# Optimization experiments

Hardware: AMD Instinct MI355X
Metric: run time of the kernel (lower is better)

## Reference

```python
import jax, jax.numpy as jnp
import numpy as np
import math

B, T, D, H, DM = 2, 2048, 1024, 16, 256
DK = D // H

def setup_inputs() -> dict:
    key = jax.random.key(0)
    ks = jax.random.split(key, 13)
    s = 0.02
    return {
        "Hx": jax.random.normal(ks[0], (B, D, T, 1), jnp.float32),
        "Hf": jax.random.normal(ks[1], (B, T, D), jnp.float32),
        "Gm": jax.random.normal(ks[2], (B, T, DM), jnp.float32),
        "Wg": jax.random.normal(ks[3], (T, DM), jnp.float32) * s,
        "bg": jax.random.normal(ks[4], (T,), jnp.float32) * s,
        "Wq": jax.random.normal(ks[5], (D, 2 * D), jnp.float32) * s,
        "bq": jax.random.normal(ks[6], (D,), jnp.float32) * s,
        "Wk": jax.random.normal(ks[7], (D, 2 * D), jnp.float32) * s,
        "bk": jax.random.normal(ks[8], (D,), jnp.float32) * s,
        "Wv": jax.random.normal(ks[9], (D, D), jnp.float32) * s,
        "bv": jax.random.normal(ks[10], (D,), jnp.float32) * s,
        "Wo": jax.random.normal(ks[11], (D, D), jnp.float32) * s,
        "bo": jax.random.normal(ks[12], (D,), jnp.float32) * s,
    }

def reference(Hx, Hf, Gm, Wg, bg, Wq, bq, Wk, bk, Wv, bv, Wo, bo):
    # Hx: (B, D, T, 1) -> (B, T, D)
    hx = jnp.transpose(Hx[..., 0], (0, 2, 1))
    h_cat = jnp.concatenate([hx, Hf], axis=-1)          # (B, T, 2D)
    Q = h_cat @ Wq.T + bq                               # (B, T, D)
    K = h_cat @ Wk.T + bk
    V = hx @ Wv.T + bv
    # split heads: (B, H, T, DK)
    Q = Q.reshape(B, T, H, DK).transpose(0, 2, 1, 3)
    K = K.reshape(B, T, H, DK).transpose(0, 2, 1, 3)
    V = V.reshape(B, T, H, DK).transpose(0, 2, 1, 3)
    scores = jnp.einsum('bhqd,bhkd->bhqk', Q, K) / math.sqrt(DK)
    bias = Gm @ Wg.T + bg                                # (B, T, T)
    scores = scores + bias[:, None, :, :]
    attn = jax.nn.softmax(scores, axis=-1)
    out = jnp.einsum('bhqk,bhkd->bhqd', attn, V)
    out = out.transpose(0, 2, 1, 3).reshape(B, T, D)
    return out @ Wo.T + bo
```

## Files before the change

### kernel.cpp

```cpp
#include <hip/hip_runtime.h>
#include <hip/hip_bf16.h>

using bf16 = __hip_bfloat16;
typedef __attribute__((ext_vector_type(8))) __bf16 bf16x8;
typedef __attribute__((ext_vector_type(4))) float f32x4;

#define GLB_AS(p) ((const __attribute__((address_space(1))) unsigned int*)(p))
#define LDS_AS(p) ((__attribute__((address_space(3))) unsigned int*)(p))

__device__ __forceinline__ void async_copy16(const void* g, void* l) {
  __builtin_amdgcn_global_load_lds(GLB_AS(g), LDS_AS(l), 16, 0, 0);
}

__device__ __forceinline__ f32x4 mfma16x16x32(bf16x8 a, bf16x8 b, f32x4 c) {
  return __builtin_amdgcn_mfma_f32_16x16x32_bf16(a, b, c, 0, 0, 0);
}

__device__ __forceinline__ float bfu2f(unsigned short u) {
  union { unsigned int i; float f; } x;
  x.i = (unsigned int)u << 16;
  return x.f;
}

#define LOG2E 1.44269504f

__global__ __launch_bounds__(256) void pack_hx(const float* __restrict__ Hx,
                                               bf16* __restrict__ hcat) {
  __shared__ float tile[64][65];
  const int t0 = blockIdx.x * 64, d0 = blockIdx.y * 64, b = blockIdx.z;
  const int c = threadIdx.x & 63, r0 = threadIdx.x >> 6;
#pragma unroll
  for (int i = 0; i < 16; ++i) {
    const int rd = r0 + i * 4;
    tile[rd][c] = Hx[((size_t)(b * 1024 + d0 + rd)) * 2048 + t0 + c];
  }
  __syncthreads();
#pragma unroll
  for (int i = 0; i < 16; ++i) {
    const int ct = r0 + i * 4;
    hcat[((size_t)(b * 2048 + t0 + ct)) * 2048 + d0 + c] =
        __float2bfloat16(tile[c][ct]);
  }
}

__global__ __launch_bounds__(256) void pack_all(
    const float* __restrict__ Hf, const float* __restrict__ Wq,
    const float* __restrict__ Wk, const float* __restrict__ Wv,
    const float* __restrict__ Wo, const float* __restrict__ Wg,
    const float* __restrict__ Gm, const float* __restrict__ bq,
    const float* __restrict__ bk, const float* __restrict__ bv,
    bf16* __restrict__ hcat, bf16* __restrict__ Wqkvb, bf16* __restrict__ Wob,
    bf16* __restrict__ Wgb, bf16* __restrict__ Gmb,
    float* __restrict__ qkvbias) {
  const int gid = blockIdx.x * 256 + threadIdx.x;
  const float* src = nullptr;
  bf16* dst = nullptr;
  int lg = 0, ldo = 0, off = 0, idx = 0;
  bool zero = false;
  if (gid < 1048576) { idx = gid; src = Hf; dst = hcat; lg = 8; ldo = 2048; off = 1024; }
  else if (gid < 1572864) { idx = gid - 1048576; src = Wq; dst = Wqkvb; lg = 9; ldo = 2048; }
  else if (gid < 2097152) { idx = gid - 1572864; src = Wk; dst = Wqkvb + (size_t)1024 * 2048; lg = 9; ldo = 2048; }
  else if (gid < 2359296) { idx = gid - 2097152; src = Wv; dst = Wqkvb + (size_t)2048 * 2048; lg = 8; ldo = 2048; }
  else if (gid < 2621440) { idx = gid - 2359296; zero = true; dst = Wqkvb + (size_t)2048 * 2048 + 1024; lg = 8; ldo = 2048; }
  else if (gid < 2883584) { idx = gid - 2621440; src = Wo; dst = Wob; lg = 8; ldo = 1024; }
  else if (gid < 3014656) { idx = gid - 2883584; src = Wg; dst = Wgb; lg = 6; ldo = 256; }
  else if (gid < 3276800) { idx = gid - 3014656; src = Gm; dst = Gmb; lg = 6; ldo = 256; }
  else if (gid < 3277056) { const int i = gid - 3276800; ((float4*)qkvbias)[i] = ((const float4*)bq)[i]; return; }
  else if (gid < 3277312) { const int i = gid - 3277056; ((float4*)(qkvbias + 1024))[i] = ((const float4*)bk)[i]; return; }
  else { const int i = gid - 3277312; ((float4*)(qkvbias + 2048))[i] = ((const float4*)bv)[i]; return; }
  const int row = idx >> lg, c = idx & ((1 << lg) - 1);
  bf16* o = dst + (size_t)row * ldo + off + c * 4;
  __align__(8) bf16 tmp[4];
  if (zero) {
    tmp[0] = tmp[1] = tmp[2] = tmp[3] = __float2bfloat16(0.f);
  } else {
    const float4 v = ((const float4*)src)[(size_t)idx];
    tmp[0] = __float2bfloat16(v.x); tmp[1] = __float2bfloat16(v.y);
    tmp[2] = __float2bfloat16(v.z); tmp[3] = __float2bfloat16(v.w);
  }
  *(ushort4*)o = *(const ushort4*)tmp;
}

__global__ __launch_bounds__(256) void gemm_qkv_bias(
    const bf16* __restrict__ hcat, const bf16* __restrict__ Wqkv,
    const float* __restrict__ qkvbias, const bf16* __restrict__ Gmb,
    const bf16* __restrict__ Wgb, const float* __restrict__ bg,
    bf16* __restrict__ QKb, bf16* __restrict__ Vt, bf16* __restrict__ biasS) {
  __shared__ __align__(16) bf16 As[128 * 64];
  __shared__ __align__(16) bf16 Bs[128 * 64];
  const bool isqkv = blockIdx.x < 24;
  const bf16* A = isqkv ? hcat : Gmb;
  const bf16* W = isqkv ? Wqkv : Wgb;
  const float* biasv = isqkv ? qkvbias : bg;
  const int Kd = isqkv ? 2048 : 256;
  const int n0 = (isqkv ? blockIdx.x : (blockIdx.x - 24)) * 128;
  const int m0 = blockIdx.y * 128;
  const int tid = threadIdx.x, lane = tid & 63, w = tid >> 6;
  const int wm = (w >> 1) * 64, wn = (w & 1) * 64;
  const int fr = lane & 15;
  const int ck = lane >> 4;

  f32x4 acc[4][4];
  const f32x4 fzero = {0.f, 0.f, 0.f, 0.f};
#pragma unroll
  for (int i = 0; i < 4; ++i)
#pragma unroll
    for (int j = 0; j < 4; ++j) acc[i][j] = fzero;

  for (int k0 = 0; k0 < Kd; k0 += 64) {
    __syncthreads();
#pragma unroll
    for (int is = 0; is < 4; ++is) {
      const int off = is * 4096 + w * 1024;
      const int row = (off >> 7) + (lane >> 3);
      const int sch = ((lane & 7) ^ (row & 7)) * 8;
      async_copy16(A + (size_t)(m0 + row) * Kd + k0 + sch, (char*)As + off);
      async_copy16(W + (size_t)(n0 + row) * Kd + k0 + sch, (char*)Bs + off);
    }
    __syncthreads();
#pragma unroll
    for (int ks = 0; ks < 2; ++ks) {
      bf16x8 af[4], bfr[4];
#pragma unroll
      for (int i = 0; i < 4; ++i) {
        const int swk = (((ks * 4 + ck) ^ (fr & 7))) * 8;
        af[i] = *(const bf16x8*)(As + (wm + i * 16 + fr) * 64 + swk);
        bfr[i] = *(const bf16x8*)(Bs + (wn + i * 16 + fr) * 64 + swk);
      }
#pragma unroll
      for (int i = 0; i < 4; ++i)
#pragma unroll
        for (int j = 0; j < 4; ++j)
          acc[i][j] = mfma16x16x32(af[i], bfr[j], acc[i][j]);
    }
  }
  const int erow = (lane >> 4) * 4;
  const int ecol = lane & 15;

  if (!isqkv) {
#pragma unroll
    for (int i = 0; i < 4; ++i) {
      const int gm0 = m0 + wm + i * 16 + erow;
#pragma unroll
      for (int j = 0; j < 4; ++j) {
        const int gn = n0 + wn + j * 16 + ecol;
        const float bv = biasv[gn];
#pragma unroll
        for (int r = 0; r < 4; ++r)
          biasS[(size_t)(gm0 + r) * 2048 + gn] =
              __float2bfloat16((acc[i][j][r] + bv) * LOG2E);
      }
    }
  } else if (n0 < 2048) {
    const float sc = (n0 < 1024) ? 0.125f * LOG2E : 1.0f;
#pragma unroll
    for (int i = 0; i < 4; ++i) {
      const int gm0 = m0 + wm + i * 16 + erow;
#pragma unroll
      for (int j = 0; j < 4; ++j) {
        const int gn = n0 + wn + j * 16 + ecol;
        const float bv = biasv[gn];
#pragma unroll
        for (int r = 0; r < 4; ++r)
          QKb[(size_t)(gm0 + r) * 2048 + gn] =
              __float2bfloat16((acc[i][j][r] + bv) * sc);
      }
    }
  } else {
#pragma unroll
    for (int i = 0; i < 4; ++i) {
      const int gm0 = m0 + wm + i * 16 + erow;
      const int bb = gm0 >> 11;
      const int t = gm0 & 2047;
#pragma unroll
      for (int j = 0; j < 4; ++j) {
        const int gn = n0 + wn + j * 16 + ecol;
        const float bv = biasv[gn];
        const int d = gn - 2048;
        __align__(8) bf16 tmp[4];
#pragma unroll
        for (int r = 0; r < 4; ++r)
          tmp[r] = __float2bfloat16(acc[i][j][r] + bv);
        *(ushort4*)(Vt + ((size_t)(bb * 1024 + d)) * 2048 + t) =
            *(const ushort4*)tmp;
      }
    }
  }
}

__global__ __launch_bounds__(256) void gemm_out(const bf16* __restrict__ A,
                                                const bf16* __restrict__ W,
                                                const float* __restrict__ biasv,
                                                float* __restrict__ C) {
  __shared__ __align__(16) bf16 As[128 * 64];
  __shared__ __align__(16) bf16 Bs[64 * 64];
  const int tid = threadIdx.x, lane = tid & 63, w = tid >> 6;
  const int m0 = blockIdx.y * 128, n0 = blockIdx.x * 64;
  const int wm = (w >> 1) * 64, wn = (w & 1) * 32;
  const int fr = lane & 15;
  const int ck = lane >> 4;

  f32x4 acc[4][2];
  const f32x4 fzero = {0.f, 0.f, 0.f, 0.f};
#pragma unroll
  for (int i = 0; i < 4; ++i)
#pragma unroll
    for (int j = 0; j < 2; ++j) acc[i][j] = fzero;

  for (int k0 = 0; k0 < 1024; k0 += 64) {
    __syncthreads();
#pragma unroll
    for (int is = 0; is < 4; ++is) {
      const int off = is * 4096 + w * 1024;
      const int row = (off >> 7) + (lane >> 3);
      const int sch = ((lane & 7) ^ (row & 7)) * 8;
      async_copy16(A + (size_t)(m0 + row) * 1024 + k0 + sch, (char*)As + off);
      if (is < 2)
        async_copy16(W + (size_t)(n0 + row) * 1024 + k0 + sch, (char*)Bs + off);
    }
    __syncthreads();
#pragma unroll
    for (int ks = 0; ks < 2; ++ks) {
      bf16x8 af[4], bfr[2];
      const int swk0 = (((ks * 4 + ck) ^ (fr & 7))) * 8;
#pragma unroll
      for (int i = 0; i < 4; ++i)
        af[i] = *(const bf16x8*)(As + (wm + i * 16 + fr) * 64 + swk0);
#pragma unroll
      for (int j = 0; j < 2; ++j)
        bfr[j] = *(const bf16x8*)(Bs + (wn + j * 16 + fr) * 64 + swk0);
#pragma unroll
      for (int i = 0; i < 4; ++i)
#pragma unroll
        for (int j = 0; j < 2; ++j)
          acc[i][j] = mfma16x16x32(af[i], bfr[j], acc[i][j]);
    }
  }
  const int erow = (lane >> 4) * 4;
  const int ecol = lane & 15;
#pragma unroll
  for (int i = 0; i < 4; ++i) {
    const int gm0 = m0 + wm + i * 16 + erow;
#pragma unroll
    for (int j = 0; j < 2; ++j) {
      const int gn = n0 + wn + j * 16 + ecol;
      const float bv = biasv[gn];
#pragma unroll
      for (int r = 0; r < 4; ++r)
        C[(size_t)(gm0 + r) * 1024 + gn] = acc[i][j][r] + bv;
    }
  }
}

__global__ __launch_bounds__(256) void flash_attn(
    const bf16* __restrict__ Qm, const bf16* __restrict__ Km,
    const bf16* __restrict__ Vtm, const bf16* __restrict__ biasS,
    bf16* __restrict__ Om) {
  __shared__ __align__(16) bf16 Ks[128 * 64];
  __shared__ __align__(16) bf16 Vs[64 * 128];
  __shared__ __align__(16) bf16 Ps[4 * 32 * 80];
  const int tid = threadIdx.x, lane = tid & 63, w = tid >> 6;
  const int q0 = blockIdx.x * 128;
  const int h = blockIdx.y, b = blockIdx.z;
  const int ql = lane & 15, qk = lane >> 4;
  const int T = 2048, D = 1024;

  bf16x8 qf[2][2];
#pragma unroll
  for (int qt = 0; qt < 2; ++qt)
#pragma unroll
    for (int ks = 0; ks < 2; ++ks)
      qf[qt][ks] = *(const bf16x8*)(
          Qm + (size_t)(b * T + q0 + w * 32 + qt * 16 + ql) * 2048 + h * 64 +
          ks * 32 + qk * 8);

  f32x4 acc[4][2];
  const f32x4 fzero = {0.f, 0.f, 0.f, 0.f};
#pragma unroll
  for (int dt = 0; dt < 4; ++dt)
#pragma unroll
    for (int qt = 0; qt < 2; ++qt) acc[dt][qt] = fzero;
  float lp[2] = {0.f, 0.f};

  const bf16* kbase = Km + (size_t)(b * T) * 2048 + h * 64;
  const bf16* vbase = Vtm + (size_t)(b * D + h * 64) * 2048;
  const bf16* bb0 = biasS + (size_t)(b * T + q0 + w * 32 + ql) * 2048 + qk * 4;
  bf16* pb = Ps + w * 2560;

  for (int j = 0; j < 16; ++j) {
    __syncthreads();
#pragma unroll
    for (int is = 0; is < 4; ++is) {
      const int off = is * 4096 + w * 1024;
      const int krow = (off >> 7) + (lane >> 3);
      const int ksch = ((lane & 7) ^ (krow & 7)) * 8;
      async_copy16(kbase + (size_t)(j * 128 + krow) * 2048 + ksch,
                   (char*)Ks + off);
      const int vrow = (off >> 8) + (lane >> 4);
      const int vsch = ((lane & 15) ^ (vrow & 15)) * 8;
      async_copy16(vbase + (size_t)vrow * 2048 + j * 128 + vsch,
                   (char*)Vs + off);
    }
    ushort4 bq[2][2][4];
#pragma unroll
    for (int jj = 0; jj < 2; ++jj)
#pragma unroll
      for (int qt = 0; qt < 2; ++qt)
#pragma unroll
        for (int jt = 0; jt < 4; ++jt)
          bq[jj][qt][jt] = *(const ushort4*)(bb0 + (size_t)qt * 16 * 2048 +
                                             j * 128 + jj * 64 + jt * 16);
    __syncthreads();
#pragma unroll
    for (int jj = 0; jj < 2; ++jj) {
#pragma unroll
      for (int jt = 0; jt < 4; ++jt) {
        const int krow = jj * 64 + jt * 16 + ql;
        const bf16x8 kf0 =
            *(const bf16x8*)(Ks + krow * 64 + ((qk ^ (ql & 7)) * 8));
        const bf16x8 kf1 =
            *(const bf16x8*)(Ks + krow * 64 + (((qk + 4) ^ (ql & 7)) * 8));
#pragma unroll
        for (int qt = 0; qt < 2; ++qt) {
          f32x4 c;
          c[0] = bfu2f(bq[jj][qt][jt].x); c[1] = bfu2f(bq[jj][qt][jt].y);
          c[2] = bfu2f(bq[jj][qt][jt].z); c[3] = bfu2f(bq[jj][qt][jt].w);
          c = mfma16x16x32(kf0, qf[qt][0], c);
          c = mfma16x16x32(kf1, qf[qt][1], c);
          __align__(8) bf16 t4[4];
#pragma unroll
          for (int r = 0; r < 4; ++r) {
            const float pv = __builtin_amdgcn_exp2f(c[r]);
            lp[qt] += pv;
            t4[r] = __float2bfloat16(pv);
          }
          *(ushort4*)(pb + (qt * 16 + ql) * 80 + jt * 16 + qk * 4) =
              *(const ushort4*)t4;
        }
      }
#pragma unroll
      for (int ks = 0; ks < 2; ++ks) {
        const bf16x8 pf0 = *(const bf16x8*)(pb + ql * 80 + ks * 32 + qk * 8);
        const bf16x8 pf1 =
            *(const bf16x8*)(pb + (16 + ql) * 80 + ks * 32 + qk * 8);
        const int vc = ((jj * 8 + ks * 4 + qk) ^ ql) * 8;
#pragma unroll
        for (int dt = 0; dt < 4; ++dt) {
          const bf16x8 vf = *(const bf16x8*)(Vs + (dt * 16 + ql) * 128 + vc);
          acc[dt][0] = mfma16x16x32(pf0, vf, acc[dt][0]);
          acc[dt][1] = mfma16x16x32(pf1, vf, acc[dt][1]);
        }
      }
    }
  }
#pragma unroll
  for (int qt = 0; qt < 2; ++qt) {
    lp[qt] += __shfl_xor(lp[qt], 16);
    lp[qt] += __shfl_xor(lp[qt], 32);
  }
  float inv[2][4];
#pragma unroll
  for (int qt = 0; qt < 2; ++qt)
#pragma unroll
    for (int r = 0; r < 4; ++r)
      inv[qt][r] = __builtin_amdgcn_rcpf(__shfl(lp[qt], qk * 4 + r));
#pragma unroll
  for (int qt = 0; qt < 2; ++qt)
#pragma unroll
    for (int r = 0; r < 4; ++r) {
      const size_t orow = (size_t)(b * T + q0 + w * 32 + qt * 16 + qk * 4 + r);
#pragma unroll
      for (int dt = 0; dt < 4; ++dt)
        Om[orow * D + h * 64 + dt * 16 + ql] =
            __float2bfloat16(acc[dt][qt][r] * inv[qt][r]);
    }
}

extern "C" void kernel_launch(void* const* d_in, const int* in_sizes, int n_in,
                              void* d_out, int out_size, void* d_ws,
                              size_t ws_size, hipStream_t stream) {
  (void)in_sizes; (void)n_in; (void)out_size; (void)ws_size;
  const float* Hx = (const float*)d_in[0];
  const float* Hf = (const float*)d_in[1];
  const float* Gm = (const float*)d_in[2];
  const float* Wg = (const float*)d_in[3];
  const float* bg = (const float*)d_in[4];
  const float* Wq = (const float*)d_in[5];
  const float* bq = (const float*)d_in[6];
  const float* Wk = (const float*)d_in[7];
  const float* bk = (const float*)d_in[8];
  const float* Wv = (const float*)d_in[9];
  const float* bv = (const float*)d_in[10];
  const float* Wo = (const float*)d_in[11];
  const float* bo = (const float*)d_in[12];
  float* out = (float*)d_out;

  char* p = (char*)d_ws;
  bf16* hcat = (bf16*)p;   p += (size_t)4096 * 2048 * 2;
  bf16* QKb = (bf16*)p;    p += (size_t)4096 * 2048 * 2;
  bf16* Vtb = (bf16*)p;    p += (size_t)4096 * 1024 * 2;
  bf16* biasS = (bf16*)p;  p += (size_t)4096 * 2048 * 2;
  bf16* AOut = (bf16*)p;   p += (size_t)4096 * 1024 * 2;
  bf16* Wqkvb = (bf16*)p;  p += (size_t)3072 * 2048 * 2;
  bf16* Wob = (bf16*)p;    p += (size_t)1024 * 1024 * 2;
  bf16* Wgb = (bf16*)p;    p += (size_t)2048 * 256 * 2;
  bf16* Gmb = (bf16*)p;    p += (size_t)4096 * 256 * 2;
  float* qkvbias = (float*)p; p += (size_t)3072 * 4;

  pack_hx<<<dim3(32, 16, 2), 256, 0, stream>>>(Hx, hcat);
  pack_all<<<dim3(12803), 256, 0, stream>>>(Hf, Wq, Wk, Wv, Wo, Wg, Gm, bq, bk,
                                            bv, hcat, Wqkvb, Wob, Wgb, Gmb,
                                            qkvbias);
  gemm_qkv_bias<<<dim3(40, 32), 256, 0, stream>>>(hcat, Wqkvb, qkvbias, Gmb,
                                                  Wgb, bg, QKb, Vtb, biasS);
  flash_attn<<<dim3(16, 16, 2), 256, 0, stream>>>(QKb, QKb + 1024, Vtb, biasS,
                                                  AOut);
  gemm_out<<<dim3(16, 32), 256, 0, stream>>>(AOut, Wob, bo, out);
}
```

Before: 301.5 us.

## Double-buffer LDS tiles in GEMMs and flash attention to overlap loads

Converts the QKV/bias GEMM, the output GEMM and the flash-attention kernel to double-buffered shared-memory tiles. The next K-tile (and, in attention, the next K/V block and bias values) is issued asynchronously while the current one is consumed, and each iteration ends with a single barrier. Flash attention shrinks its KV block from 128 to 64 keys so the two buffers fit in LDS, and it prefetches bias into registers. The aim is to hide global-load latency behind MFMA work, at the cost of more LDS per block (possibly lower occupancy), more registers and twice as many attention loop iterations.

```diff
diff --git a/kernel.cpp b/kernel.cpp
--- a/kernel.cpp
+++ b/kernel.cpp
@@ -86,8 +86,8 @@
     const float* __restrict__ qkvbias, const bf16* __restrict__ Gmb,
     const bf16* __restrict__ Wgb, const float* __restrict__ bg,
     bf16* __restrict__ QKb, bf16* __restrict__ Vt, bf16* __restrict__ biasS) {
-  __shared__ __align__(16) bf16 As[128 * 64];
-  __shared__ __align__(16) bf16 Bs[128 * 64];
+  __shared__ __align__(16) bf16 As[2][128 * 64];
+  __shared__ __align__(16) bf16 Bs[2][128 * 64];
   const bool isqkv = blockIdx.x < 24;
   const bf16* A = isqkv ? hcat : Gmb;
   const bf16* W = isqkv ? Wqkv : Wgb;
@@ -107,25 +107,34 @@
 #pragma unroll
     for (int j = 0; j < 4; ++j) acc[i][j] = fzero;
 
-  for (int k0 = 0; k0 < Kd; k0 += 64) {
-    __syncthreads();
+  auto stage = [&](int it, int buf) {
+    const int k0 = it * 64;
 #pragma unroll
     for (int is = 0; is < 4; ++is) {
       const int off = is * 4096 + w * 1024;
       const int row = (off >> 7) + (lane >> 3);
       const int sch = ((lane & 7) ^ (row & 7)) * 8;
-      async_copy16(A + (size_t)(m0 + row) * Kd + k0 + sch, (char*)As + off);
-      async_copy16(W + (size_t)(n0 + row) * Kd + k0 + sch, (char*)Bs + off);
-    }
-    __syncthreads();
+      async_copy16(A + (size_t)(m0 + row) * Kd + k0 + sch,
+                   (char*)As[buf] + off);
+      async_copy16(W + (size_t)(n0 + row) * Kd + k0 + sch,
+                   (char*)Bs[buf] + off);
+    }
+  };
+
+  const int nit = Kd >> 6;
+  stage(0, 0);
+  __syncthreads();
+  for (int it = 0; it < nit; ++it) {
+    const int cur = it & 1;
+    if (it + 1 < nit) stage(it + 1, cur ^ 1);
 #pragma unroll
     for (int ks = 0; ks < 2; ++ks) {
       bf16x8 af[4], bfr[4];
 #pragma unroll
       for (int i = 0; i < 4; ++i) {
         const int swk = (((ks * 4 + ck) ^ (fr & 7))) * 8;
-        af[i] = *(const bf16x8*)(As + (wm + i * 16 + fr) * 64 + swk);
-        bfr[i] = *(const bf16x8*)(Bs + (wn + i * 16 + fr) * 64 + swk);
+        af[i] = *(const bf16x8*)(As[cur] + (wm + i * 16 + fr) * 64 + swk);
+        bfr[i] = *(const bf16x8*)(Bs[cur] + (wn + i * 16 + fr) * 64 + swk);
       }
 #pragma unroll
       for (int i = 0; i < 4; ++i)
@@ -133,6 +142,7 @@
         for (int j = 0; j < 4; ++j)
           acc[i][j] = mfma16x16x32(af[i], bfr[j], acc[i][j]);
     }
+    __syncthreads();
   }
   const int erow = (lane >> 4) * 4;
   const int ecol = lane & 15;
@@ -192,8 +202,8 @@
                                                 const bf16* __restrict__ W,
                                                 const float* __restrict__ biasv,
                                                 float* __restrict__ C) {
-  __shared__ __align__(16) bf16 As[128 * 64];
-  __shared__ __align__(16) bf16 Bs[64 * 64];
+  __shared__ __align__(16) bf16 As[2][128 * 64];
+  __shared__ __align__(16) bf16 Bs[2][64 * 64];
   const int tid = threadIdx.x, lane = tid & 63, w = tid >> 6;
   const int m0 = blockIdx.y * 128, n0 = blockIdx.x * 64;
   const int wm = (w >> 1) * 64, wn = (w & 1) * 32;
@@ -207,34 +217,43 @@
 #pragma unroll
     for (int j = 0; j < 2; ++j) acc[i][j] = fzero;
 
-  for (int k0 = 0; k0 < 1024; k0 += 64) {
-    __syncthreads();
+  auto stage = [&](int it, int buf) {
+    const int k0 = it * 64;
 #pragma unroll
     for (int is = 0; is < 4; ++is) {
       const int off = is * 4096 + w * 1024;
       const int row = (off >> 7) + (lane >> 3);
       const int sch = ((lane & 7) ^ (row & 7)) * 8;
-      async_copy16(A + (size_t)(m0 + row) * 1024 + k0 + sch, (char*)As + off);
+      async_copy16(A + (size_t)(m0 + row) * 1024 + k0 + sch,
+                   (char*)As[buf] + off);
       if (is < 2)
-        async_copy16(W + (size_t)(n0 + row) * 1024 + k0 + sch, (char*)Bs + off);
-    }
-    __syncthreads();
+        async_copy16(W + (size_t)(n0 + row) * 1024 + k0 + sch,
+                     (char*)Bs[buf] + off);
+    }
+  };
+
+  stage(0, 0);
+  __syncthreads();
+  for (int it = 0; it < 16; ++it) {
+    const int cur = it & 1;
+    if (it + 1 < 16) stage(it + 1, cur ^ 1);
 #pragma unroll
     for (int ks = 0; ks < 2; ++ks) {
       bf16x8 af[4], bfr[2];
       const int swk0 = (((ks * 4 + ck) ^ (fr & 7))) * 8;
 #pragma unroll
       for (int i = 0; i < 4; ++i)
-        af[i] = *(const bf16x8*)(As + (wm + i * 16 + fr) * 64 + swk0);
+        af[i] = *(const bf16x8*)(As[cur] + (wm + i * 16 + fr) * 64 + swk0);
 #pragma unroll
       for (int j = 0; j < 2; ++j)
-        bfr[j] = *(const bf16x8*)(Bs + (wn + j * 16 + fr) * 64 + swk0);
+        bfr[j] = *(const bf16x8*)(Bs[cur] + (wn + j * 16 + fr) * 64 + swk0);
 #pragma unroll
       for (int i = 0; i < 4; ++i)
 #pragma unroll
         for (int j = 0; j < 2; ++j)
           acc[i][j] = mfma16x16x32(af[i], bfr[j], acc[i][j]);
     }
+    __syncthreads();
   }
   const int erow = (lane >> 4) * 4;
   const int ecol = lane & 15;
@@ -256,14 +275,16 @@
     const bf16* __restrict__ Qm, const bf16* __restrict__ Km,
     const bf16* __restrict__ Vtm, const bf16* __restrict__ biasS,
     bf16* __restrict__ Om) {
-  __shared__ __align__(16) bf16 Ks[128 * 64];
-  __shared__ __align__(16) bf16 Vs[64 * 128];
+  __shared__ __align__(16) bf16 Ks[2][64 * 64];
+  __shared__ __align__(16) bf16 Vs[2][64 * 64];
   __shared__ __align__(16) bf16 Ps[4 * 32 * 80];
   const int tid = threadIdx.x, lane = tid & 63, w = tid >> 6;
   const int q0 = blockIdx.x * 128;
   const int h = blockIdx.y, b = blockIdx.z;
   const int ql = lane & 15, qk = lane >> 4;
   const int T = 2048, D = 1024;
+  const int sw0 = (qk ^ (ql & 7)) * 8;
+  const int sw1 = ((qk + 4) ^ (ql & 7)) * 8;
 
   bf16x8 qf[2][2];
 #pragma unroll
@@ -287,71 +308,83 @@
   const bf16* bb0 = biasS + (size_t)(b * T + q0 + w * 32 + ql) * 2048 + qk * 4;
   bf16* pb = Ps + w * 2560;
 
-  for (int j = 0; j < 16; ++j) {
+  auto stage = [&](int j, int buf) {
+#pragma unroll
+    for (int is = 0; is < 2; ++is) {
+      const int off = is * 4096 + w * 1024;
+      const int row = (off >> 7) + (lane >> 3);
+      const int sch = ((lane & 7) ^ (row & 7)) * 8;
+      async_copy16(kbase + (size_t)(j * 64 + row) * 2048 + sch,
+                   (char*)Ks[buf] + off);
+      async_copy16(vbase + (size_t)row * 2048 + j * 64 + sch,
+                   (char*)Vs[buf] + off);
+    }
+  };
+
+  ushort4 bq[2][4], bqn[2][4];
+  stage(0, 0);
+#pragma unroll
+  for (int qt = 0; qt < 2; ++qt)
+#pragma unroll
+    for (int jt = 0; jt < 4; ++jt)
+      bq[qt][jt] = *(const ushort4*)(bb0 + (size_t)qt * 16 * 2048 + jt * 16);
+  __syncthreads();
+
+  for (int j = 0; j < 32; ++j) {
+    const int cur = j & 1;
+    if (j < 31) {
+      stage(j + 1, cur ^ 1);
+#pragma unroll
+      for (int qt = 0; qt < 2; ++qt)
+#pragma unroll
+        for (int jt = 0; jt < 4; ++jt)
+          bqn[qt][jt] = *(const ushort4*)(bb0 + (size_t)qt * 16 * 2048 +
+                                          (j + 1) * 64 + jt * 16);
+    }
+    const bf16* ksp = Ks[cur];
+    const bf16* vsp = Vs[cur];
+#pragma unroll
+    for (int jt = 0; jt < 4; ++jt) {
+      const bf16x8 kf0 = *(const bf16x8*)(ksp + (jt * 16 + ql) * 64 + sw0);
+      const bf16x8 kf1 = *(const bf16x8*)(ksp + (jt * 16 + ql) * 64 + sw1);
+#pragma unroll
+      for (int qt = 0; qt < 2; ++qt) {
+        f32x4 c;
+        c[0] = bfu2f(bq[qt][jt].x); c[1] = bfu2f(bq[qt][jt].y);
+        c[2] = bfu2f(bq[qt][jt].z); c[3] = bfu2f(bq[qt][jt].w);
+        c = mfma16x16x32(kf0, qf[qt][0], c);
+        c = mfma16x16x32(kf1, qf[qt][1], c);
+        __align__(8) bf16 t4[4];
+#pragma unroll
+        for (int r = 0; r < 4; ++r) {
+          const float pv = __builtin_amdgcn_exp2f(c[r]);
+          lp[qt] += pv;
+          t4[r] = __float2bfloat16(pv);
+        }
+        *(ushort4*)(pb + (qt * 16 + ql) * 80 + jt * 16 + qk * 4) =
+            *(const ushort4*)t4;
+      }
+    }
+#pragma unroll
+    for (int ks = 0; ks < 2; ++ks) {
+      const bf16x8 pf0 = *(const bf16x8*)(pb + ql * 80 + ks * 32 + qk * 8);
+      const bf16x8 pf1 =
+          *(const bf16x8*)(pb + (16 + ql) * 80 + ks * 32 + qk * 8);
+      const int sw = ks ? sw1 : sw0;
+#pragma unroll
+      for (int dt = 0; dt < 4; ++dt) {
+        const bf16x8 vf = *(const bf16x8*)(vsp + (dt * 16 + ql) * 64 + sw);
+        acc[dt][0] = mfma16x16x32(pf0, vf, acc[dt][0]);
+        acc[dt][1] = mfma16x16x32(pf1, vf, acc[dt][1]);
+      }
+    }
+    if (j < 31) {
+#pragma unroll
+      for (int qt = 0; qt < 2; ++qt)
+#pragma unroll
+        for (int jt = 0; jt < 4; ++jt) bq[qt][jt] = bqn[qt][jt];
+    }
     __syncthreads();
-#pragma unroll
-    for (int is = 0; is < 4; ++is) {
-      const int off = is * 4096 + w * 1024;
-      const int krow = (off >> 7) + (lane >> 3);
-      const int ksch = ((lane & 7) ^ (krow & 7)) * 8;
-      async_copy16(kbase + (size_t)(j * 128 + krow) * 2048 + ksch,
-                   (char*)Ks + off);
-      const int vrow = (off >> 8) + (lane >> 4);
-      const int vsch = ((lane & 15) ^ (vrow & 15)) * 8;
-      async_copy16(vbase + (size_t)vrow * 2048 + j * 128 + vsch,
-                   (char*)Vs + off);
-    }
-    ushort4 bq[2][2][4];
-#pragma unroll
-    for (int jj = 0; jj < 2; ++jj)
-#pragma unroll
-      for (int qt = 0; qt < 2; ++qt)
-#pragma unroll
-        for (int jt = 0; jt < 4; ++jt)
-          bq[jj][qt][jt] = *(const ushort4*)(bb0 + (size_t)qt * 16 * 2048 +
-                                             j * 128 + jj * 64 + jt * 16);
-    __syncthreads();
-#pragma unroll
-    for (int jj = 0; jj < 2; ++jj) {
-#pragma unroll
-      for (int jt = 0; jt < 4; ++jt) {
-        const int krow = jj * 64 + jt * 16 + ql;
-        const bf16x8 kf0 =
-            *(const bf16x8*)(Ks + krow * 64 + ((qk ^ (ql & 7)) * 8));
-        const bf16x8 kf1 =
-            *(const bf16x8*)(Ks + krow * 64 + (((qk + 4) ^ (ql & 7)) * 8));
-#pragma unroll
-        for (int qt = 0; qt < 2; ++qt) {
-          f32x4 c;
-          c[0] = bfu2f(bq[jj][qt][jt].x); c[1] = bfu2f(bq[jj][qt][jt].y);
-          c[2] = bfu2f(bq[jj][qt][jt].z); c[3] = bfu2f(bq[jj][qt][jt].w);
-          c = mfma16x16x32(kf0, qf[qt][0], c);
-          c = mfma16x16x32(kf1, qf[qt][1], c);
-          __align__(8) bf16 t4[4];
-#pragma unroll
-          for (int r = 0; r < 4; ++r) {
-            const float pv = __builtin_amdgcn_exp2f(c[r]);
-            lp[qt] += pv;
-            t4[r] = __float2bfloat16(pv);
-          }
-          *(ushort4*)(pb + (qt * 16 + ql) * 80 + jt * 16 + qk * 4) =
-              *(const ushort4*)t4;
-        }
-      }
-#pragma unroll
-      for (int ks = 0; ks < 2; ++ks) {
-        const bf16x8 pf0 = *(const bf16x8*)(pb + ql * 80 + ks * 32 + qk * 8);
-        const bf16x8 pf1 =
-            *(const bf16x8*)(pb + (16 + ql) * 80 + ks * 32 + qk * 8);
-        const int vc = ((jj * 8 + ks * 4 + qk) ^ ql) * 8;
-#pragma unroll
-        for (int dt = 0; dt < 4; ++dt) {
-          const bf16x8 vf = *(const bf16x8*)(Vs + (dt * 16 + ql) * 128 + vc);
-          acc[dt][0] = mfma16x16x32(pf0, vf, acc[dt][0]);
-          acc[dt][1] = mfma16x16x32(pf1, vf, acc[dt][1]);
-        }
-      }
-    }
   }
 #pragma unroll
   for (int qt = 0; qt < 2; ++qt) {
```

Result: no change. 298.9 us (-0.9%).
